# Kernel optimization log

Hardware: AMD Instinct MI355X
Metric: run time of the kernel (lower is better)

The kernel has to match this reference:

```python
import jax, jax.numpy as jnp
import numpy as np

B, O, T, C_IN, IMG, P, D = 16, 3, 8, 3, 224, 16, 768
HF = IMG // P  # 14x14 conv feature grid
S = 7          # ObjectsCrops output size (SxS per object per frame)


def setup_inputs() -> dict:
    key = jax.random.key(0)
    ks = jax.random.split(key, 6)
    x = jax.random.normal(ks[0], (B, C_IN, T, IMG, IMG), dtype=jnp.float32)
    # metadata: [B, O, T, 4] boxes (x1,y1,x2,y2) in pixel coords within [0,224]
    u = jax.random.uniform(ks[1], (B, O, T, 4), dtype=jnp.float32)
    bx1 = u[..., 0] * 160.0
    by1 = u[..., 1] * 160.0
    bw = 16.0 + u[..., 2] * 48.0
    bh = 16.0 + u[..., 3] * 48.0
    metadata = jnp.stack([bx1, by1, jnp.minimum(bx1 + bw, 224.0), jnp.minimum(by1 + bh, 224.0)], axis=-1)
    proj_w = jax.random.normal(ks[2], (D, C_IN, P, P), dtype=jnp.float32) * 0.02  # Conv3d kernel, tubelet dim (=1) squeezed
    proj_b = jnp.zeros((D,), dtype=jnp.float32)
    box_categories = jax.random.normal(ks[3], (T, O, D), dtype=jnp.float32) * 0.02
    w1 = jax.random.normal(ks[4], (4, D // 2), dtype=jnp.float32) * 0.1   # Linear(4, 384, bias=False)
    w2 = jax.random.normal(ks[5], (D // 2, D), dtype=jnp.float32) * 0.05  # Linear(384, 768, bias=False)
    return dict(x=x, metadata=metadata, proj_w=proj_w, proj_b=proj_b, box_categories=box_categories, w1=w1, w2=w2)


def _roi_crop(feat, boxes):
    # feat: [BT, C, Hf, Wf]; boxes: [BT, O, 4] (x1,y1,x2,y2) in feature-map coords
    BT, C, Hf, Wf = feat.shape
    x1, y1, x2, y2 = (boxes[..., i] for i in range(4))
    cell = (jnp.arange(S, dtype=feat.dtype) + 0.5) / S               # sample cell centers
    ys = y1[..., None] + cell * (y2 - y1)[..., None]                 # [BT,O,S]
    xs = x1[..., None] + cell * (x2 - x1)[..., None]
    yg = jnp.broadcast_to(ys[:, :, :, None], (BT, O, S, S)) - 0.5    # pixel centers at idx+0.5
    xg = jnp.broadcast_to(xs[:, :, None, :], (BT, O, S, S)) - 0.5
    y0f = jnp.floor(yg); x0f = jnp.floor(xg)
    wy = yg - y0f; wx = xg - x0f
    y0 = jnp.clip(y0f.astype(jnp.int32), 0, Hf - 1); y1i = jnp.clip(y0 + 1, 0, Hf - 1)
    x0 = jnp.clip(x0f.astype(jnp.int32), 0, Wf - 1); x1i = jnp.clip(x0 + 1, 0, Wf - 1)
    gather = jax.vmap(lambda fm, yy, xx: fm[:, yy, xx])              # [C,Hf,Wf],[O,S,S] -> [C,O,S,S]
    v00 = gather(feat, y0, x0); v01 = gather(feat, y0, x1i)
    v10 = gather(feat, y1i, x0); v11 = gather(feat, y1i, x1i)
    wy = wy[:, None]; wx = wx[:, None]                               # [BT,1,O,S,S]
    return (v00 * (1 - wy) * (1 - wx) + v01 * (1 - wy) * wx
            + v10 * wy * (1 - wx) + v11 * wy * wx)                   # [BT,C,O,S,S]


def reference(x, metadata, proj_w, proj_b, box_categories, w1, w2):
    Bs = x.shape[0]
    boxes = jnp.transpose(metadata, (0, 2, 1, 3))                    # [B,T,O,4] pixel coords
    # coordinate MLP on normalized boxes + per-(frame,object) category embedding
    box_emb = jax.nn.relu(jax.nn.relu((boxes / 224.0) @ w1) @ w2)    # [B,T,O,D]
    box_emb = box_categories[None] + box_emb
    # Conv3d patch embed: tubelet=1, stride==kernel -> non-overlapping patchify + GEMM
    xp = x.reshape(Bs, C_IN, T, HF, P, HF, P)
    feat = jnp.einsum('bcthpwq,dcpq->btdhw', xp, proj_w) + proj_b[None, None, :, None, None]
    feat = feat.reshape(Bs * T, D, HF, HF)
    fboxes = boxes.reshape(Bs * T, O, 4) * (HF / 224.0)              # boxes in feature coords
    crops = _roi_crop(feat, fboxes).reshape(Bs, T, D, O, S, S)
    xo = jnp.transpose(crops, (0, 3, 2, 1, 4, 5))                    # [B,O,C,T,S,S]
    emb = jnp.transpose(box_emb, (0, 2, 3, 1))                       # [B,O,D,T]
    xo = xo + emb[..., None, None]
    xo = xo.reshape(Bs * O, D, T, S * S)                             # flatten(3) on [N*O,C,T,H,W]
    return jnp.transpose(xo, (0, 2, 3, 1))                           # [B*O, T, S*S, D]
```

## Files before the change

### kernel.cpp

```cpp
#include <hip/hip_runtime.h>
#include <hip/hip_bf16.h>

typedef unsigned int u32;
typedef unsigned short ushort_t;
typedef __bf16 bf16x8 __attribute__((ext_vector_type(8)));
typedef float f32x4 __attribute__((ext_vector_type(4)));
typedef unsigned short ushort8 __attribute__((ext_vector_type(8)));

#define BB 16
#define OO 3
#define TT 8
#define CIN 3
#define IMG 224
#define PP 16
#define DD 768
#define HFD 14
#define SS 7
#define GM 25088
#define GK 768
#define GN 768

__device__ __forceinline__ ushort_t f2bf(float f) {
    u32 u = __float_as_uint(f);
    u32 r = (u + 0x7FFFu + ((u >> 16) & 1u)) >> 16;
    return (ushort_t)r;
}

__device__ __forceinline__ void load_lds16(const void* g, void* l) {
    __builtin_amdgcn_global_load_lds(
        (const __attribute__((address_space(1))) u32*)g,
        (__attribute__((address_space(3))) u32*)l, 16, 0, 0);
}

__global__ __launch_bounds__(256) void pack_a(const float* __restrict__ x,
                                              ushort_t* __restrict__ Ap) {
    int g = blockIdx.x * 256 + threadIdx.x;
    int m = g / 96;
    int k0 = (g % 96) * 8;
    int w = m % 14;
    int h = (m / 14) % 14;
    int t = (m / 196) % 8;
    int b = m / 1568;
    int c = k0 >> 8;
    int rem = k0 & 255;
    int p = rem >> 4;
    int q0 = rem & 15;
    const float* src = x + ((((size_t)(b * 3 + c) * 8 + t) * 224 + (h * 16 + p)) * 224
                            + (w * 16 + q0));
    f32x4 f0 = *(const f32x4*)src;
    f32x4 f1 = *(const f32x4*)(src + 4);
    ushort8 r;
    r[0] = f2bf(f0[0]); r[1] = f2bf(f0[1]); r[2] = f2bf(f0[2]); r[3] = f2bf(f0[3]);
    r[4] = f2bf(f1[0]); r[5] = f2bf(f1[1]); r[6] = f2bf(f1[2]); r[7] = f2bf(f1[3]);
    *(ushort8*)(Ap + (size_t)m * 768 + k0) = r;
}

__global__ __launch_bounds__(256) void pack_w(const float* __restrict__ w,
                                              ushort_t* __restrict__ Wp) {
    size_t g = ((size_t)blockIdx.x * 256 + threadIdx.x) * 8;
    f32x4 f0 = *(const f32x4*)(w + g);
    f32x4 f1 = *(const f32x4*)(w + g + 4);
    ushort8 r;
    r[0] = f2bf(f0[0]); r[1] = f2bf(f0[1]); r[2] = f2bf(f0[2]); r[3] = f2bf(f0[3]);
    r[4] = f2bf(f1[0]); r[5] = f2bf(f1[1]); r[6] = f2bf(f1[2]); r[7] = f2bf(f1[3]);
    *(ushort8*)(Wp + g) = r;
}

__global__ __launch_bounds__(256) void box_mlp(const float* __restrict__ meta,
                                               const float* __restrict__ w1,
                                               const float* __restrict__ w2,
                                               const float* __restrict__ cats,
                                               float* __restrict__ emb) {
    int bt = blockIdx.x;
    int b = bt / 8, t = bt % 8;
    __shared__ float H[3][384];
    int tid = threadIdx.x;
    for (int idx = tid; idx < 3 * 384; idx += 256) {
        int o = idx / 384, j = idx % 384;
        const float* mp = meta + ((b * 3 + o) * 8 + t) * 4;
        float s = 0.f;
        #pragma unroll
        for (int i = 0; i < 4; ++i) s += (mp[i] * (1.0f / 224.0f)) * w1[i * 384 + j];
        H[o][j] = fmaxf(s, 0.f);
    }
    __syncthreads();
    float acc[3][3] = {};
    for (int j = 0; j < 384; ++j) {
        float w0 = w2[j * 768 + tid];
        float w1v = w2[j * 768 + tid + 256];
        float w2v = w2[j * 768 + tid + 512];
        #pragma unroll
        for (int o = 0; o < 3; ++o) {
            float h = H[o][j];
            acc[o][0] += h * w0;
            acc[o][1] += h * w1v;
            acc[o][2] += h * w2v;
        }
    }
    #pragma unroll
    for (int o = 0; o < 3; ++o)
        #pragma unroll
        for (int c = 0; c < 3; ++c) {
            int d = tid + c * 256;
            emb[((size_t)(b * 8 + t) * 3 + o) * 768 + d] =
                fmaxf(acc[o][c], 0.f) + cats[(t * 3 + o) * 768 + d];
        }
}

__global__ __launch_bounds__(256) void gemm_bt(const ushort_t* __restrict__ A,
                                               const ushort_t* __restrict__ Bt,
                                               const float* __restrict__ pb,
                                               float* __restrict__ C) {
    __shared__ ushort_t lA[128 * 64];
    __shared__ ushort_t lB[128 * 64];
    int tid = threadIdx.x;
    int bm = blockIdx.x % 196;
    int bn = blockIdx.x / 196;
    size_t m0 = (size_t)bm * 128, n0 = (size_t)bn * 128;
    int w = tid >> 6, lane = tid & 63;
    int wr = w >> 1, wc = w & 1;

    f32x4 acc[4][4] = {};

    for (int kt = 0; kt < 12; ++kt) {
        int k0 = kt * 64;
        __syncthreads();
        #pragma unroll
        for (int r = 0; r < 4; ++r) {
            int cidx = r * 256 + tid;
            int row = cidx >> 3;
            int col = (cidx & 7) * 8;
            load_lds16(A + ((m0 + row) * 768 + k0 + col), &lA[(size_t)cidx * 8]);
        }
        #pragma unroll
        for (int r = 0; r < 4; ++r) {
            int cidx = r * 256 + tid;
            int row = cidx >> 3;
            int col = (cidx & 7) * 8;
            load_lds16(Bt + ((n0 + row) * 768 + k0 + col), &lB[(size_t)cidx * 8]);
        }
        __syncthreads();
        #pragma unroll
        for (int kk = 0; kk < 2; ++kk) {
            bf16x8 af[4], bfr[4];
            #pragma unroll
            for (int mi = 0; mi < 4; ++mi)
                af[mi] = *(const bf16x8*)&lA[(wr * 64 + mi * 16 + (lane & 15)) * 64
                                             + kk * 32 + (lane >> 4) * 8];
            #pragma unroll
            for (int ni = 0; ni < 4; ++ni)
                bfr[ni] = *(const bf16x8*)&lB[(wc * 64 + ni * 16 + (lane & 15)) * 64
                                              + kk * 32 + (lane >> 4) * 8];
            #pragma unroll
            for (int mi = 0; mi < 4; ++mi)
                #pragma unroll
                for (int ni = 0; ni < 4; ++ni)
                    acc[mi][ni] = __builtin_amdgcn_mfma_f32_16x16x32_bf16(
                        af[mi], bfr[ni], acc[mi][ni], 0, 0, 0);
        }
    }

    int rbase = (lane >> 4) * 4;
    int cl = lane & 15;
    #pragma unroll
    for (int ni = 0; ni < 4; ++ni) {
        size_t col = n0 + wc * 64 + ni * 16 + cl;
        float pbv = pb[col];
        #pragma unroll
        for (int mi = 0; mi < 4; ++mi) {
            size_t row = m0 + wr * 64 + mi * 16 + rbase;
            #pragma unroll
            for (int j = 0; j < 4; ++j) {
                C[(row + j) * 768 + col] = acc[mi][ni][j] + pbv;
            }
        }
    }
}

__global__ __launch_bounds__(192) void roi_kernel(const float* __restrict__ meta,
                                                  const float* __restrict__ feat,
                                                  const float* __restrict__ emb,
                                                  float* __restrict__ out) {
    int id = blockIdx.x;
    int i = id % 7; id /= 7;
    int o = id % 3; id /= 3;
    int t = id % 8;
    int b = id / 8;

    const float* mp = meta + ((b * 3 + o) * 8 + t) * 4;
    float x1 = mp[0] * (1.f / 16.f);
    float y1 = mp[1] * (1.f / 16.f);
    float x2 = mp[2] * (1.f / 16.f);
    float y2 = mp[3] * (1.f / 16.f);

    float ci = (i + 0.5f) * (1.f / 7.f);
    float yg = y1 + ci * (y2 - y1) - 0.5f;
    float y0f = floorf(yg);
    float wy = yg - y0f;
    int y0 = min(max((int)y0f, 0), 13);
    int y1c = min(y0 + 1, 13);

    int bt = b * 8 + t;
    const float* fbase = feat + (size_t)bt * 196 * 768;
    const float* ep = emb + ((size_t)(b * 8 + t) * 3 + o) * 768;

    int d = threadIdx.x * 4;
    f32x4 ev = *(const f32x4*)(ep + d);

    for (int j = 0; j < 7; ++j) {
        float cj = (j + 0.5f) * (1.f / 7.f);
        float xgv = x1 + cj * (x2 - x1) - 0.5f;
        float x0f = floorf(xgv);
        float wx = xgv - x0f;
        int x0 = min(max((int)x0f, 0), 13);
        int x1i = min(x0 + 1, 13);

        f32x4 v00 = *(const f32x4*)(fbase + ((size_t)y0 * 14 + x0) * 768 + d);
        f32x4 v01 = *(const f32x4*)(fbase + ((size_t)y0 * 14 + x1i) * 768 + d);
        f32x4 v10 = *(const f32x4*)(fbase + ((size_t)y1c * 14 + x0) * 768 + d);
        f32x4 v11 = *(const f32x4*)(fbase + ((size_t)y1c * 14 + x1i) * 768 + d);

        float w00 = (1.f - wy) * (1.f - wx);
        float w01 = (1.f - wy) * wx;
        float w10 = wy * (1.f - wx);
        float w11 = wy * wx;

        f32x4 r;
        #pragma unroll
        for (int e = 0; e < 4; ++e)
            r[e] = v00[e] * w00 + v01[e] * w01 + v10[e] * w10 + v11[e] * w11 + ev[e];

        int pp = i * 7 + j;
        *(f32x4*)(out + ((((size_t)(b * 3 + o) * 8 + t) * 49 + pp) * 768 + d)) = r;
    }
}

extern "C" void kernel_launch(void* const* d_in, const int* in_sizes, int n_in,
                              void* d_out, int out_size, void* d_ws, size_t ws_size,
                              hipStream_t stream) {
    const float* x     = (const float*)d_in[0];
    const float* meta  = (const float*)d_in[1];
    const float* projw = (const float*)d_in[2];
    const float* projb = (const float*)d_in[3];
    const float* cats  = (const float*)d_in[4];
    const float* w1    = (const float*)d_in[5];
    const float* w2    = (const float*)d_in[6];
    float* out = (float*)d_out;

    char* ws = (char*)d_ws;
    const size_t szA   = (size_t)GM * GK * 2;
    const size_t szW   = (size_t)GN * GK * 2;
    const size_t szF   = (size_t)GM * GN * 4;
    ushort_t* Ap  = (ushort_t*)(ws);
    ushort_t* Wp  = (ushort_t*)(ws + szA);
    float*    feat = (float*)(ws + szA + szW);
    float*    emb  = (float*)(ws + szA + szW + szF);

    pack_a<<<9408, 256, 0, stream>>>(x, Ap);
    pack_w<<<288, 256, 0, stream>>>(projw, Wp);
    box_mlp<<<128, 256, 0, stream>>>(meta, w1, w2, cats, emb);
    gemm_bt<<<196 * 6, 256, 0, stream>>>(Ap, Wp, projb, feat);
    roi_kernel<<<16 * 8 * 3 * 7, 192, 0, stream>>>(meta, feat, emb, out);
}
```

Measured before the change: 273.0 us.

## Coalesce pack_a reads, split box MLP across blocks, XCD-aware block remapping

pack_a now walks the input image contiguously, with each thread reading 16 consecutive floats and writing two bf16 vectors. This replaces the strided patch-order reads. box_mlp is split three ways along D so it launches more blocks, each computing one output column per thread. The GEMM and ROI kernels remap block IDs so consecutive work lands on the same XCD (bid&7 interleave), aiming for better L2 reuse of shared A/B tiles and feature maps. The pack_a writes become more scattered, and the remap depends on the round-robin XCD dispatch assumption.

```diff
diff --git a/kernel.cpp b/kernel.cpp
--- a/kernel.cpp
+++ b/kernel.cpp
@@ -7,15 +7,6 @@
 typedef float f32x4 __attribute__((ext_vector_type(4)));
 typedef unsigned short ushort8 __attribute__((ext_vector_type(8)));
 
-#define BB 16
-#define OO 3
-#define TT 8
-#define CIN 3
-#define IMG 224
-#define PP 16
-#define DD 768
-#define HFD 14
-#define SS 7
 #define GM 25088
 #define GK 768
 #define GN 768
@@ -35,24 +26,30 @@
 __global__ __launch_bounds__(256) void pack_a(const float* __restrict__ x,
                                               ushort_t* __restrict__ Ap) {
     int g = blockIdx.x * 256 + threadIdx.x;
-    int m = g / 96;
-    int k0 = (g % 96) * 8;
-    int w = m % 14;
-    int h = (m / 14) % 14;
-    int t = (m / 196) % 8;
-    int b = m / 1568;
-    int c = k0 >> 8;
-    int rem = k0 & 255;
-    int p = rem >> 4;
-    int q0 = rem & 15;
-    const float* src = x + ((((size_t)(b * 3 + c) * 8 + t) * 224 + (h * 16 + p)) * 224
-                            + (w * 16 + q0));
+    int w = g % 14;
+    int rowg = g / 14;
+    int row = rowg % 224;
+    int bct = rowg / 224;
+    int t = bct % 8;
+    int bc = bct / 8;
+    int c = bc % 3;
+    int b = bc / 3;
+    int p = row & 15;
+    int h = row >> 4;
+    const float* src = x + (size_t)g * 16;
     f32x4 f0 = *(const f32x4*)src;
     f32x4 f1 = *(const f32x4*)(src + 4);
-    ushort8 r;
-    r[0] = f2bf(f0[0]); r[1] = f2bf(f0[1]); r[2] = f2bf(f0[2]); r[3] = f2bf(f0[3]);
-    r[4] = f2bf(f1[0]); r[5] = f2bf(f1[1]); r[6] = f2bf(f1[2]); r[7] = f2bf(f1[3]);
-    *(ushort8*)(Ap + (size_t)m * 768 + k0) = r;
+    f32x4 f2 = *(const f32x4*)(src + 8);
+    f32x4 f3 = *(const f32x4*)(src + 12);
+    ushort8 r0, r1;
+    r0[0] = f2bf(f0[0]); r0[1] = f2bf(f0[1]); r0[2] = f2bf(f0[2]); r0[3] = f2bf(f0[3]);
+    r0[4] = f2bf(f1[0]); r0[5] = f2bf(f1[1]); r0[6] = f2bf(f1[2]); r0[7] = f2bf(f1[3]);
+    r1[0] = f2bf(f2[0]); r1[1] = f2bf(f2[1]); r1[2] = f2bf(f2[2]); r1[3] = f2bf(f2[3]);
+    r1[4] = f2bf(f3[0]); r1[5] = f2bf(f3[1]); r1[6] = f2bf(f3[2]); r1[7] = f2bf(f3[3]);
+    int m = ((b * 8 + t) * 14 + h) * 14 + w;
+    int k = c * 256 + p * 16;
+    *(ushort8*)(Ap + (size_t)m * 768 + k) = r0;
+    *(ushort8*)(Ap + (size_t)m * 768 + k + 8) = r1;
 }
 
 __global__ __launch_bounds__(256) void pack_w(const float* __restrict__ w,
@@ -71,7 +68,8 @@
                                                const float* __restrict__ w2,
                                                const float* __restrict__ cats,
                                                float* __restrict__ emb) {
-    int bt = blockIdx.x;
+    int bt = blockIdx.x / 3;
+    int dc = blockIdx.x % 3;
     int b = bt / 8, t = bt % 8;
     __shared__ float H[3][384];
     int tid = threadIdx.x;
@@ -84,27 +82,20 @@
         H[o][j] = fmaxf(s, 0.f);
     }
     __syncthreads();
-    float acc[3][3] = {};
+    int d = dc * 256 + tid;
+    float acc[3] = {0.f, 0.f, 0.f};
+    #pragma unroll 4
     for (int j = 0; j < 384; ++j) {
-        float w0 = w2[j * 768 + tid];
-        float w1v = w2[j * 768 + tid + 256];
-        float w2v = w2[j * 768 + tid + 512];
-        #pragma unroll
-        for (int o = 0; o < 3; ++o) {
-            float h = H[o][j];
-            acc[o][0] += h * w0;
-            acc[o][1] += h * w1v;
-            acc[o][2] += h * w2v;
-        }
+        float wv = w2[j * 768 + d];
+        acc[0] += H[0][j] * wv;
+        acc[1] += H[1][j] * wv;
+        acc[2] += H[2][j] * wv;
     }
     #pragma unroll
-    for (int o = 0; o < 3; ++o)
-        #pragma unroll
-        for (int c = 0; c < 3; ++c) {
-            int d = tid + c * 256;
-            emb[((size_t)(b * 8 + t) * 3 + o) * 768 + d] =
-                fmaxf(acc[o][c], 0.f) + cats[(t * 3 + o) * 768 + d];
-        }
+    for (int o = 0; o < 3; ++o) {
+        emb[((size_t)bt * 3 + o) * 768 + d] =
+            fmaxf(acc[o], 0.f) + cats[(t * 3 + o) * 768 + d];
+    }
 }
 
 __global__ __launch_bounds__(256) void gemm_bt(const ushort_t* __restrict__ A,
@@ -114,8 +105,10 @@
     __shared__ ushort_t lA[128 * 64];
     __shared__ ushort_t lB[128 * 64];
     int tid = threadIdx.x;
-    int bm = blockIdx.x % 196;
-    int bn = blockIdx.x / 196;
+    int bid = blockIdx.x;
+    int wid = (bid & 7) * 147 + (bid >> 3);
+    int bm = wid / 6;
+    int bn = wid % 6;
     size_t m0 = (size_t)bm * 128, n0 = (size_t)bn * 128;
     int w = tid >> 6, lane = tid & 63;
     int wr = w >> 1, wc = w & 1;
@@ -181,11 +174,12 @@
                                                   const float* __restrict__ feat,
                                                   const float* __restrict__ emb,
                                                   float* __restrict__ out) {
-    int id = blockIdx.x;
-    int i = id % 7; id /= 7;
-    int o = id % 3; id /= 3;
-    int t = id % 8;
-    int b = id / 8;
+    int bid = blockIdx.x;
+    int wid = (bid & 7) * 336 + (bid >> 3);
+    int i = wid % 7; wid /= 7;
+    int o = wid % 3; wid /= 3;
+    int t = wid % 8;
+    int b = wid / 8;
 
     const float* mp = meta + ((b * 3 + o) * 8 + t) * 4;
     float x1 = mp[0] * (1.f / 16.f);
@@ -202,7 +196,7 @@
 
     int bt = b * 8 + t;
     const float* fbase = feat + (size_t)bt * 196 * 768;
-    const float* ep = emb + ((size_t)(b * 8 + t) * 3 + o) * 768;
+    const float* ep = emb + ((size_t)bt * 3 + o) * 768;
 
     int d = threadIdx.x * 4;
     f32x4 ev = *(const f32x4*)(ep + d);
@@ -248,17 +242,17 @@
     float* out = (float*)d_out;
 
     char* ws = (char*)d_ws;
-    const size_t szA   = (size_t)GM * GK * 2;
-    const size_t szW   = (size_t)GN * GK * 2;
-    const size_t szF   = (size_t)GM * GN * 4;
-    ushort_t* Ap  = (ushort_t*)(ws);
-    ushort_t* Wp  = (ushort_t*)(ws + szA);
+    const size_t szA = (size_t)GM * GK * 2;
+    const size_t szW = (size_t)GN * GK * 2;
+    const size_t szF = (size_t)GM * GN * 4;
+    ushort_t* Ap   = (ushort_t*)(ws);
+    ushort_t* Wp   = (ushort_t*)(ws + szA);
     float*    feat = (float*)(ws + szA + szW);
     float*    emb  = (float*)(ws + szA + szW + szF);
 
-    pack_a<<<9408, 256, 0, stream>>>(x, Ap);
+    pack_a<<<4704, 256, 0, stream>>>(x, Ap);
     pack_w<<<288, 256, 0, stream>>>(projw, Wp);
-    box_mlp<<<128, 256, 0, stream>>>(meta, w1, w2, cats, emb);
-    gemm_bt<<<196 * 6, 256, 0, stream>>>(Ap, Wp, projb, feat);
-    roi_kernel<<<16 * 8 * 3 * 7, 192, 0, stream>>>(meta, feat, emb, out);
-}
+    box_mlp<<<128 * 3, 256, 0, stream>>>(meta, w1, w2, cats, emb);
+    gemm_bt<<<1176, 256, 0, stream>>>(Ap, Wp, projb, feat);
+    roi_kernel<<<2688, 192, 0, stream>>>(meta, feat, emb, out);
+}
```

Measured after the change: 270.5 us. No clear change (-0.9%).
